# Kernel optimization log

Hardware: AMD Instinct MI355X
Metric: run time of the kernel (lower is better)

Reference implementation:

```python
import jax, jax.numpy as jnp
import numpy as np

N = 100000
E = 800000
HID = 128
HEADS = 4
NEG_SLOPE = 0.2


def _mlp2(x, w1, b1, w2, b2):
    h = jax.nn.relu(x @ w1.T + b1)
    return jax.nn.relu(h @ w2.T + b2)


def gat_conv(h, src, dst, lin_w, att_src, att_dst, bias, heads, out_ch, concat):
    # h: [N, in] -> hl: [N, heads, out_ch]
    n = h.shape[0]
    hl = (h @ lin_w.T).reshape(n, heads, out_ch)
    a_s = jnp.sum(hl * att_src, axis=-1)  # [N, heads]
    a_d = jnp.sum(hl * att_dst, axis=-1)
    alpha = jax.nn.leaky_relu(a_s[src] + a_d[dst], NEG_SLOPE)  # [E', heads]
    amax = jax.ops.segment_max(alpha, dst, num_segments=n)
    ex = jnp.exp(alpha - amax[dst])
    denom = jax.ops.segment_sum(ex, dst, num_segments=n)
    att = ex / denom[dst]  # segment softmax over incoming edges
    msg = hl[src] * att[:, :, None]  # [E', heads, out_ch]
    out = jax.ops.segment_sum(msg, dst, num_segments=n)
    out = out.reshape(n, heads * out_ch) if concat else out.mean(axis=1)
    return out + bias


def setup_inputs() -> dict:
    key = jax.random.key(0)
    ks = iter(jax.random.split(key, 40))
    g = lambda shape: (jax.random.normal(next(ks), shape, dtype=jnp.float32) * 0.1)
    inp = {}
    inp['x'] = jax.random.normal(next(ks), (N, 2), dtype=jnp.float32)
    inp['node_types'] = jax.random.randint(next(ks), (N,), 0, 2, dtype=jnp.int32)
    inp['edge_index'] = jax.random.randint(next(ks), (2, E), 0, N, dtype=jnp.int64)
    # heterogeneous encoder
    inp['ew1'] = g((HID, 2)); inp['eb1'] = g((HID,))
    inp['ew2'] = g((HID, HID)); inp['eb2'] = g((HID,))
    inp['cw1'] = g((HID, 1)); inp['cb1'] = g((HID,))
    inp['cw2'] = g((HID, HID)); inp['cb2'] = g((HID,))
    # GAT layers 0,1: heads=4, out_ch=HID//4, concat
    C = HID // HEADS
    inp['lin0'] = g((HID, HID)); inp['as0'] = g((HEADS, C)); inp['ad0'] = g((HEADS, C)); inp['b0'] = g((HID,))
    inp['lin1'] = g((HID, HID)); inp['as1'] = g((HEADS, C)); inp['ad1'] = g((HEADS, C)); inp['b1'] = g((HID,))
    # GAT layer 2: heads=1, out_ch=HID, concat=False
    inp['lin2'] = g((HID, HID)); inp['as2'] = g((1, HID)); inp['ad2'] = g((1, HID)); inp['b2'] = g((HID,))
    # decoder
    inp['dw1'] = g((HID, HID)); inp['db1'] = g((HID,))
    inp['dw2'] = g((HID // 2, HID)); inp['db2'] = g((HID // 2,))
    inp['dw3'] = g((1, HID // 2)); inp['db3'] = g((1,))
    return inp


def reference(x, node_types, edge_index, ew1, eb1, ew2, eb2, cw1, cb1, cw2, cb2,
              lin0, as0, ad0, b0, lin1, as1, ad1, b1, lin2, as2, ad2, b2,
              dw1, db1, dw2, db2, dw3, db3):
    n = x.shape[0]
    # heterogeneous encoding (vectorized type select)
    item_h = _mlp2(x[:, :2], ew1, eb1, ew2, eb2)
    con_h = _mlp2(x[:, :1], cw1, cb1, cw2, cb2)
    item_mask = node_types == 0
    h = jnp.where(item_mask[:, None], item_h, jnp.where((node_types == 1)[:, None], con_h, 0.0))
    # add self-loops (PyG GATConv default add_self_loops=True)
    loop = jnp.arange(n, dtype=edge_index.dtype)
    src = jnp.concatenate([edge_index[0], loop])
    dst = jnp.concatenate([edge_index[1], loop])
    C = HID // HEADS
    h0 = jax.nn.relu(gat_conv(h, src, dst, lin0, as0, ad0, b0, HEADS, C, True))
    h1 = h0 + jax.nn.relu(gat_conv(h0, src, dst, lin1, as1, ad1, b1, HEADS, C, True))
    h2 = h1 + jax.nn.relu(gat_conv(h1, src, dst, lin2, as2, ad2, b2, 1, HID, False))
    # decoder on all nodes; zero out non-item nodes (dropout is eval/no-op)
    d = jax.nn.relu(h2 @ dw1.T + db1)
    d = jax.nn.relu(d @ dw2.T + db2)
    probs = jax.nn.sigmoid(d @ dw3.T + db3).squeeze(-1)
    return probs * item_mask.astype(probs.dtype)
```

## Files before the change

kernel.cpp:

```cpp
#include <hip/hip_runtime.h>
#include <math.h>

#define HIDDEN 128
#define NEG_SLOPE 0.2f

typedef unsigned short u16;
typedef __attribute__((ext_vector_type(8))) short bf16x8;
typedef __attribute__((ext_vector_type(4))) float f32x4;

__device__ __forceinline__ u16 f2bf(float f) {
    unsigned u = __float_as_uint(f);
    unsigned r = (u + 0x7FFFu + ((u >> 16) & 1u)) >> 16;
    return (u16)r;
}
__device__ __forceinline__ float bf2f(u16 u) {
    return __uint_as_float((unsigned)u << 16);
}
__device__ __forceinline__ unsigned pack2(float a, float b) {
    return (unsigned)f2bf(a) | ((unsigned)f2bf(b) << 16);
}
__device__ __forceinline__ float lo16f(unsigned v) { return bf2f((u16)v); }
__device__ __forceinline__ float hi16f(unsigned v) { return bf2f((u16)(v >> 16)); }

struct WPtrs { const float* p[7]; };
__global__ void convw_zero_kernel(WPtrs wp, unsigned* __restrict__ wb, int totalPairs,
                                  int* __restrict__ cnt, int N) {
    int i = blockIdx.x * blockDim.x + threadIdx.x;
    if (i < N) cnt[i] = 0;
    if (i < totalPairs) {
        int e = i * 2;
        int seg, off;
        if (e < 98304) { seg = e >> 14; off = e & 16383; }
        else           { seg = 6;       off = e - 98304; }
        const float* s = wp.p[seg];
        wb[i] = pack2(s[off], s[off + 1]);
    }
}

__global__ __launch_bounds__(256) void encoder_kernel(
        const float* __restrict__ x, const int* __restrict__ types,
        const float* __restrict__ ew1, const float* __restrict__ eb1,
        const float* __restrict__ cw1, const float* __restrict__ cb1,
        const u16* __restrict__ wb_ew2, const u16* __restrict__ wb_cw2,
        const float* __restrict__ eb2, const float* __restrict__ cb2,
        u16* __restrict__ out, int N) {
    __shared__ u16 Ws[128 * 136];
    __shared__ float xsh[128];
    __shared__ float w1sh[640];
    const int tid = threadIdx.x;
    const int n0 = blockIdx.x * 64;

    if (tid < 128) {
        int n = n0 + (tid >> 1);
        xsh[tid] = (n < N) ? x[2 * n + (tid & 1)] : 0.f;
    }
    if (tid < 256) w1sh[tid] = ew1[tid];
    if (tid < 128) { w1sh[256 + tid] = eb1[tid]; w1sh[384 + tid] = cw1[tid];
                     w1sh[512 + tid] = cb1[tid]; }
#pragma unroll
    for (int r = 0; r < 8; r++) {
        int j = r * 256 + tid;
        int row = j >> 4, c8 = (j & 15) << 3;
        *(uint4*)&Ws[row * 136 + c8] = *(const uint4*)&wb_ew2[(size_t)row * 128 + c8];
    }
    __syncthreads();

    const int w = tid >> 6, lane = tid & 63;
    const int qd = lane >> 4, lr = lane & 15;
    const int arow = w * 16 + lr;
    const float x0 = xsh[2 * arow], x1 = xsh[2 * arow + 1];

    f32x4 acc_i[8], acc_c[8];
#pragma unroll
    for (int j = 0; j < 8; j++) acc_i[j] = (f32x4){0.f, 0.f, 0.f, 0.f};

#pragma unroll
    for (int k = 0; k < 4; k++) {
        bf16x8 a;
#pragma unroll
        for (int j = 0; j < 8; j++) {
            int t = k * 32 + qd * 8 + j;
            float v = fmaxf(w1sh[2 * t] * x0 + w1sh[2 * t + 1] * x1 + w1sh[256 + t], 0.f);
            a[j] = (short)f2bf(v);
        }
#pragma unroll
        for (int j = 0; j < 8; j++) {
            bf16x8 b = *(const bf16x8*)&Ws[(j * 16 + lr) * 136 + k * 32 + qd * 8];
            acc_i[j] = __builtin_amdgcn_mfma_f32_16x16x32_bf16(a, b, acc_i[j], 0, 0, 0);
        }
    }
    __syncthreads();

#pragma unroll
    for (int r = 0; r < 8; r++) {
        int j = r * 256 + tid;
        int rw = j >> 4, c8 = (j & 15) << 3;
        *(uint4*)&Ws[rw * 136 + c8] = *(const uint4*)&wb_cw2[(size_t)rw * 128 + c8];
    }
    __syncthreads();

#pragma unroll
    for (int j = 0; j < 8; j++) acc_c[j] = (f32x4){0.f, 0.f, 0.f, 0.f};
#pragma unroll
    for (int k = 0; k < 4; k++) {
        bf16x8 a;
#pragma unroll
        for (int j = 0; j < 8; j++) {
            int t = k * 32 + qd * 8 + j;
            float v = fmaxf(w1sh[384 + t] * x0 + w1sh[512 + t], 0.f);
            a[j] = (short)f2bf(v);
        }
#pragma unroll
        for (int j = 0; j < 8; j++) {
            bf16x8 b = *(const bf16x8*)&Ws[(j * 16 + lr) * 136 + k * 32 + qd * 8];
            acc_c[j] = __builtin_amdgcn_mfma_f32_16x16x32_bf16(a, b, acc_c[j], 0, 0, 0);
        }
    }

#pragma unroll
    for (int r = 0; r < 4; r++) {
        int orow = n0 + w * 16 + qd * 4 + r;
        if (orow >= N) continue;
        int ty = types[orow];
#pragma unroll
        for (int j = 0; j < 8; j++) {
            int col = j * 16 + lr;
            float v;
            if (ty == 0)      v = fmaxf(acc_i[j][r] + eb2[col], 0.f);
            else if (ty == 1) v = fmaxf(acc_c[j][r] + cb2[col], 0.f);
            else              v = 0.f;
            out[(size_t)orow * HIDDEN + col] = f2bf(v);
        }
    }
}

template <int DH>
__global__ __launch_bounds__(256) void gemm_hl_kernel(
        const u16* __restrict__ X, const u16* __restrict__ Wb,
        const float* __restrict__ att_s, const float* __restrict__ att_d,
        u16* __restrict__ hl, float* __restrict__ a_s, float* __restrict__ a_d,
        int N) {
    __shared__ u16 Xs[64 * 136];
    __shared__ u16 Ws[128 * 136];
    const int tid = threadIdx.x;
    const int n0 = blockIdx.x * 64;

#pragma unroll
    for (int r = 0; r < 4; r++) {
        int j = r * 256 + tid;
        int row = j >> 4, c8 = (j & 15) << 3;
        int n = n0 + row;
        uint4 v = make_uint4(0u, 0u, 0u, 0u);
        if (n < N) v = *(const uint4*)&X[(size_t)n * 128 + c8];
        *(uint4*)&Xs[row * 136 + c8] = v;
    }
#pragma unroll
    for (int r = 0; r < 8; r++) {
        int j = r * 256 + tid;
        int row = j >> 4, c8 = (j & 15) << 3;
        *(uint4*)&Ws[row * 136 + c8] = *(const uint4*)&Wb[(size_t)row * 128 + c8];
    }
    __syncthreads();

    const int w = tid >> 6, lane = tid & 63;
    const int qd = lane >> 4, lr = lane & 15;

    f32x4 acc[8];
#pragma unroll
    for (int j = 0; j < 8; j++) acc[j] = (f32x4){0.f, 0.f, 0.f, 0.f};
#pragma unroll
    for (int k = 0; k < 4; k++) {
        bf16x8 a = *(const bf16x8*)&Xs[(w * 16 + lr) * 136 + k * 32 + qd * 8];
#pragma unroll
        for (int j = 0; j < 8; j++) {
            bf16x8 b = *(const bf16x8*)&Ws[(j * 16 + lr) * 136 + k * 32 + qd * 8];
            acc[j] = __builtin_amdgcn_mfma_f32_16x16x32_bf16(a, b, acc[j], 0, 0, 0);
        }
    }

    constexpr int NH = (DH == 4) ? 4 : 1;
    float sp[NH][4], dp[NH][4];
#pragma unroll
    for (int h = 0; h < NH; h++)
#pragma unroll
        for (int r = 0; r < 4; r++) { sp[h][r] = 0.f; dp[h][r] = 0.f; }
#pragma unroll
    for (int j = 0; j < 8; j++) {
        int col = j * 16 + lr;
        float as_ = att_s[col], ad_ = att_d[col];
        int h = (DH == 4) ? (j >> 1) : 0;
#pragma unroll
        for (int r = 0; r < 4; r++) {
            sp[h][r] += acc[j][r] * as_;
            dp[h][r] += acc[j][r] * ad_;
        }
    }
#pragma unroll
    for (int m = 1; m < 16; m <<= 1)
#pragma unroll
        for (int h = 0; h < NH; h++)
#pragma unroll
            for (int r = 0; r < 4; r++) {
                sp[h][r] += __shfl_xor(sp[h][r], m, 64);
                dp[h][r] += __shfl_xor(dp[h][r], m, 64);
            }
    if (lr == 0) {
#pragma unroll
        for (int r = 0; r < 4; r++) {
            int row = n0 + w * 16 + qd * 4 + r;
            if (row < N) {
#pragma unroll
                for (int h = 0; h < NH; h++) {
                    a_s[row * DH + h] = sp[h][r];
                    a_d[row * DH + h] = dp[h][r];
                }
            }
        }
    }
#pragma unroll
    for (int r = 0; r < 4; r++) {
        int row = n0 + w * 16 + qd * 4 + r;
        if (row >= N) continue;
#pragma unroll
        for (int j = 0; j < 8; j++)
            hl[(size_t)row * 128 + j * 16 + lr] = f2bf(acc[j][r]);
    }
}

__global__ __launch_bounds__(256) void dec_kernel(
        const u16* __restrict__ X, const int* __restrict__ types,
        const u16* __restrict__ wb_dw1, const float* __restrict__ db1,
        const u16* __restrict__ wb_dw2, const float* __restrict__ db2,
        const float* __restrict__ dw3, const float* __restrict__ db3,
        float* __restrict__ fout, int N) {
    __shared__ u16 Xs[64 * 136];
    __shared__ u16 Ws[128 * 136];
    const int tid = threadIdx.x;
    const int n0 = blockIdx.x * 64;

#pragma unroll
    for (int r = 0; r < 4; r++) {
        int j = r * 256 + tid;
        int row = j >> 4, c8 = (j & 15) << 3;
        int n = n0 + row;
        uint4 v = make_uint4(0u, 0u, 0u, 0u);
        if (n < N) v = *(const uint4*)&X[(size_t)n * 128 + c8];
        *(uint4*)&Xs[row * 136 + c8] = v;
    }
#pragma unroll
    for (int r = 0; r < 8; r++) {
        int j = r * 256 + tid;
        int row = j >> 4, c8 = (j & 15) << 3;
        *(uint4*)&Ws[row * 136 + c8] = *(const uint4*)&wb_dw1[(size_t)row * 128 + c8];
    }
    __syncthreads();

    const int w = tid >> 6, lane = tid & 63;
    const int qd = lane >> 4, lr = lane & 15;

    f32x4 acc[8];
#pragma unroll
    for (int j = 0; j < 8; j++) acc[j] = (f32x4){0.f, 0.f, 0.f, 0.f};
#pragma unroll
    for (int k = 0; k < 4; k++) {
        bf16x8 a = *(const bf16x8*)&Xs[(w * 16 + lr) * 136 + k * 32 + qd * 8];
#pragma unroll
        for (int j = 0; j < 8; j++) {
            bf16x8 b = *(const bf16x8*)&Ws[(j * 16 + lr) * 136 + k * 32 + qd * 8];
            acc[j] = __builtin_amdgcn_mfma_f32_16x16x32_bf16(a, b, acc[j], 0, 0, 0);
        }
    }
    __syncthreads();

#pragma unroll
    for (int r = 0; r < 4; r++) {
        int drow = w * 16 + qd * 4 + r;
#pragma unroll
        for (int j = 0; j < 8; j++) {
            int col = j * 16 + lr;
            float v = fmaxf(acc[j][r] + db1[col], 0.f);
            float vo = __shfl_xor(v, 1, 64);
            if ((lr & 1) == 0)
                *(unsigned*)&Xs[drow * 136 + j * 16 + lr] = pack2(v, vo);
        }
    }
#pragma unroll
    for (int r = 0; r < 4; r++) {
        int j = r * 256 + tid;
        int row = j >> 4, c8 = (j & 15) << 3;
        *(uint4*)&Ws[row * 136 + c8] = *(const uint4*)&wb_dw2[(size_t)row * 128 + c8];
    }
    __syncthreads();

    f32x4 acc2[4];
#pragma unroll
    for (int j = 0; j < 4; j++) acc2[j] = (f32x4){0.f, 0.f, 0.f, 0.f};
#pragma unroll
    for (int k = 0; k < 4; k++) {
        bf16x8 a = *(const bf16x8*)&Xs[(w * 16 + lr) * 136 + k * 32 + qd * 8];
#pragma unroll
        for (int j = 0; j < 4; j++) {
            bf16x8 b = *(const bf16x8*)&Ws[(j * 16 + lr) * 136 + k * 32 + qd * 8];
            acc2[j] = __builtin_amdgcn_mfma_f32_16x16x32_bf16(a, b, acc2[j], 0, 0, 0);
        }
    }
    float pr[4] = {0.f, 0.f, 0.f, 0.f};
#pragma unroll
    for (int j = 0; j < 4; j++) {
        int col = j * 16 + lr;
        float b = db2[col], wv = dw3[col];
#pragma unroll
        for (int r = 0; r < 4; r++) pr[r] += fmaxf(acc2[j][r] + b, 0.f) * wv;
    }
#pragma unroll
    for (int m = 1; m < 16; m <<= 1)
#pragma unroll
        for (int r = 0; r < 4; r++) pr[r] += __shfl_xor(pr[r], m, 64);
    if (lr == 0) {
        float b3 = db3[0];
#pragma unroll
        for (int r = 0; r < 4; r++) {
            int row = n0 + w * 16 + qd * 4 + r;
            if (row < N) {
                float prob = 1.f / (1.f + expf(-(pr[r] + b3)));
                fout[row] = (types[row] == 0) ? prob : 0.f;
            }
        }
    }
}

__global__ void hist_kernel(const int* __restrict__ ei, int E, int E2,
                            int* __restrict__ cnt, int* __restrict__ pos) {
    int e = blockIdx.x * blockDim.x + threadIdx.x;
    if (e >= E2) return;
    int d = (e < E) ? ei[E + e] : e - E;
    pos[e] = atomicAdd(&cnt[d], 1);
}

__global__ void scan1_kernel(const int* __restrict__ cnt, int* __restrict__ rs,
                             int* __restrict__ bsum, int N) {
    __shared__ int s[256];
    int i = blockIdx.x * 256 + threadIdx.x;
    int v = (i < N) ? cnt[i] : 0;
    s[threadIdx.x] = v;
    __syncthreads();
    for (int off = 1; off < 256; off <<= 1) {
        int t = (threadIdx.x >= off) ? s[threadIdx.x - off] : 0;
        __syncthreads();
        s[threadIdx.x] += t;
        __syncthreads();
    }
    if (i < N) rs[i] = s[threadIdx.x];
    if (threadIdx.x == 255) bsum[blockIdx.x] = s[255];
}

__global__ void scan23_kernel(int* __restrict__ rs, const int* __restrict__ cnt,
                              const int* __restrict__ bsum, int N) {
    __shared__ int sdata[256];
    int b = blockIdx.x;
    int partial = 0;
    for (int i = threadIdx.x; i < b; i += 256) partial += bsum[i];
    sdata[threadIdx.x] = partial;
    __syncthreads();
    for (int off = 128; off; off >>= 1) {
        if (threadIdx.x < off) sdata[threadIdx.x] += sdata[threadIdx.x + off];
        __syncthreads();
    }
    int pre = sdata[0];
    int i = b * 256 + threadIdx.x;
    if (i < N) rs[i] = rs[i] - cnt[i] + pre;
}

__global__ void scatter_kernel(const int* __restrict__ ei, int E, int E2,
                               const int* __restrict__ rs, const int* __restrict__ pos,
                               int* __restrict__ srclist) {
    int e = blockIdx.x * blockDim.x + threadIdx.x;
    if (e >= E2) return;
    int s, d;
    if (e < E) { s = ei[e]; d = ei[E + e]; }
    else       { s = d = e - E; }
    srclist[rs[d] + pos[e]] = s;
}

template <int H>
__global__ __launch_bounds__(256) void gat_agg_kernel(
        const int* __restrict__ rs, const int* __restrict__ cnt,
        const int* __restrict__ srclist, const u16* __restrict__ hl,
        const float* __restrict__ a_s, const float* __restrict__ a_d,
        const float* __restrict__ bias, const u16* __restrict__ res,
        u16* __restrict__ out, int N) {
    int n = blockIdx.x * 4 + (threadIdx.x >> 6);
    int l = threadIdx.x & 63;
    if (n >= N) return;
    const int g = l >> 4;
    const int c = l & 15;
    const int head = (H == 1) ? 0 : (c >> 2);
    const int beg = rs[n];
    const int deg = cnt[n];
    const float ad = a_d[n * H + head];
    float acc0[8], acc1[8], acc2[8];
    float den0 = 0.f, den1 = 0.f, den2 = 0.f;
#pragma unroll
    for (int j = 0; j < 8; j++) { acc0[j] = 0.f; acc1[j] = 0.f; acc2[j] = 0.f; }

    for (int k = 0; k < deg; k += 12) {
        int i0 = k + g, i1 = k + 4 + g, i2 = k + 8 + g;
        int e0 = beg + min(i0, deg - 1);
        int e1 = beg + min(i1, deg - 1);
        int e2 = beg + min(i2, deg - 1);
        int s0 = srclist[e0], s1 = srclist[e1], s2 = srclist[e2];
        float al0 = a_s[s0 * H + head] + ad;
        float al1 = a_s[s1 * H + head] + ad;
        float al2 = a_s[s2 * H + head] + ad;
        al0 = (al0 > 0.f) ? al0 : NEG_SLOPE * al0;
        al1 = (al1 > 0.f) ? al1 : NEG_SLOPE * al1;
        al2 = (al2 > 0.f) ? al2 : NEG_SLOPE * al2;
        float p0 = __expf(fminf(al0, 80.f));
        float p1 = __expf(fminf(al1, 80.f));
        float p2 = __expf(fminf(al2, 80.f));
        if (i0 >= deg) p0 = 0.f;
        if (i1 >= deg) p1 = 0.f;
        if (i2 >= deg) p2 = 0.f;
        den0 += p0; den1 += p1; den2 += p2;
        uint4 v0 = *(const uint4*)&hl[(size_t)s0 * 128 + 8 * c];
        uint4 v1 = *(const uint4*)&hl[(size_t)s1 * 128 + 8 * c];
        uint4 v2 = *(const uint4*)&hl[(size_t)s2 * 128 + 8 * c];
        acc0[0] += p0 * lo16f(v0.x); acc0[1] += p0 * hi16f(v0.x);
        acc0[2] += p0 * lo16f(v0.y); acc0[3] += p0 * hi16f(v0.y);
        acc0[4] += p0 * lo16f(v0.z); acc0[5] += p0 * hi16f(v0.z);
        acc0[6] += p0 * lo16f(v0.w); acc0[7] += p0 * hi16f(v0.w);
        acc1[0] += p1 * lo16f(v1.x); acc1[1] += p1 * hi16f(v1.x);
        acc1[2] += p1 * lo16f(v1.y); acc1[3] += p1 * hi16f(v1.y);
        acc1[4] += p1 * lo16f(v1.z); acc1[5] += p1 * hi16f(v1.z);
        acc1[6] += p1 * lo16f(v1.w); acc1[7] += p1 * hi16f(v1.w);
        acc2[0] += p2 * lo16f(v2.x); acc2[1] += p2 * hi16f(v2.x);
        acc2[2] += p2 * lo16f(v2.y); acc2[3] += p2 * hi16f(v2.y);
        acc2[4] += p2 * lo16f(v2.z); acc2[5] += p2 * hi16f(v2.z);
        acc2[6] += p2 * lo16f(v2.w); acc2[7] += p2 * hi16f(v2.w);
    }
#pragma unroll
    for (int j = 0; j < 8; j++) {
        float a = acc0[j] + acc1[j] + acc2[j];
        a += __shfl_xor(a, 16, 64);
        a += __shfl_xor(a, 32, 64);
        acc0[j] = a;
    }
    float den = den0 + den1 + den2;
    den += __shfl_xor(den, 16, 64);
    den += __shfl_xor(den, 32, 64);
    if (g == 0) {
        float di = 1.f / den;
        float4 b0 = *(const float4*)&bias[8 * c];
        float4 b1 = *(const float4*)&bias[8 * c + 4];
        float o[8];
        o[0] = fmaxf(acc0[0] * di + b0.x, 0.f);
        o[1] = fmaxf(acc0[1] * di + b0.y, 0.f);
        o[2] = fmaxf(acc0[2] * di + b0.z, 0.f);
        o[3] = fmaxf(acc0[3] * di + b0.w, 0.f);
        o[4] = fmaxf(acc0[4] * di + b1.x, 0.f);
        o[5] = fmaxf(acc0[5] * di + b1.y, 0.f);
        o[6] = fmaxf(acc0[6] * di + b1.z, 0.f);
        o[7] = fmaxf(acc0[7] * di + b1.w, 0.f);
        if (res) {
            uint4 rv = *(const uint4*)&res[(size_t)n * 128 + 8 * c];
            o[0] += lo16f(rv.x); o[1] += hi16f(rv.x);
            o[2] += lo16f(rv.y); o[3] += hi16f(rv.y);
            o[4] += lo16f(rv.z); o[5] += hi16f(rv.z);
            o[6] += lo16f(rv.w); o[7] += hi16f(rv.w);
        }
        uint4 ov = make_uint4(pack2(o[0], o[1]), pack2(o[2], o[3]),
                              pack2(o[4], o[5]), pack2(o[6], o[7]));
        *(uint4*)&out[(size_t)n * 128 + 8 * c] = ov;
    }
}

extern "C" void kernel_launch(void* const* d_in, const int* in_sizes, int n_in,
                              void* d_out, int out_size, void* d_ws, size_t ws_size,
                              hipStream_t stream) {
    const float* x     = (const float*)d_in[0];
    const int*   types = (const int*)d_in[1];
    const int*   ei    = (const int*)d_in[2];
    const float* ew1 = (const float*)d_in[3];
    const float* eb1 = (const float*)d_in[4];
    const float* ew2 = (const float*)d_in[5];
    const float* eb2 = (const float*)d_in[6];
    const float* cw1 = (const float*)d_in[7];
    const float* cb1 = (const float*)d_in[8];
    const float* cw2 = (const float*)d_in[9];
    const float* cb2 = (const float*)d_in[10];
    const float* lin0 = (const float*)d_in[11];
    const float* as0  = (const float*)d_in[12];
    const float* ad0  = (const float*)d_in[13];
    const float* b0   = (const float*)d_in[14];
    const float* lin1 = (const float*)d_in[15];
    const float* as1  = (const float*)d_in[16];
    const float* ad1  = (const float*)d_in[17];
    const float* b1   = (const float*)d_in[18];
    const float* lin2 = (const float*)d_in[19];
    const float* as2  = (const float*)d_in[20];
    const float* ad2  = (const float*)d_in[21];
    const float* b2   = (const float*)d_in[22];
    const float* dw1 = (const float*)d_in[23];
    const float* db1 = (const float*)d_in[24];
    const float* dw2 = (const float*)d_in[25];
    const float* db2 = (const float*)d_in[26];
    const float* dw3 = (const float*)d_in[27];
    const float* db3 = (const float*)d_in[28];

    int N  = in_sizes[1];
    int E  = in_sizes[2] / 2;
    int E2 = E + N;

    size_t NF = (size_t)N * HIDDEN;
    u16* bufA = (u16*)d_ws;
    u16* bufB = bufA + NF;
    u16* bufC = bufB + NF;
    float* a_s  = (float*)(bufC + NF);
    float* a_d  = a_s + (size_t)N * 4;
    int* rs      = (int*)(a_d + (size_t)N * 4);
    int* cnt     = rs + N;
    int* pos     = cnt + N;
    int* bsum    = pos + E2;
    int* srclist = bsum + 1024;
    u16* wb      = (u16*)(srclist + E2);
    u16* wb_ew2  = wb;
    u16* wb_cw2  = wb + 16384;
    u16* wb_lin0 = wb + 32768;
    u16* wb_lin1 = wb + 49152;
    u16* wb_lin2 = wb + 65536;
    u16* wb_dw1  = wb + 81920;
    u16* wb_dw2  = wb + 98304;

    int nb = (N + 255) / 256;

    WPtrs wp;
    wp.p[0] = ew2; wp.p[1] = cw2; wp.p[2] = lin0; wp.p[3] = lin1;
    wp.p[4] = lin2; wp.p[5] = dw1; wp.p[6] = dw2;
    int cz = max(N, 53248);
    convw_zero_kernel<<<(cz + 255) / 256, 256, 0, stream>>>(wp, (unsigned*)wb, 53248,
                                                            cnt, N);

    hist_kernel<<<(E2 + 255) / 256, 256, 0, stream>>>(ei, E, E2, cnt, pos);
    scan1_kernel<<<nb, 256, 0, stream>>>(cnt, rs, bsum, N);
    scan23_kernel<<<nb, 256, 0, stream>>>(rs, cnt, bsum, N);
    scatter_kernel<<<(E2 + 255) / 256, 256, 0, stream>>>(ei, E, E2, rs, pos, srclist);

    int gx = (N + 63) / 64;

    encoder_kernel<<<gx, 256, 0, stream>>>(x, types, ew1, eb1, cw1, cb1,
                                           wb_ew2, wb_cw2, eb2, cb2, bufA, N);

    gemm_hl_kernel<4><<<gx, 256, 0, stream>>>(bufA, wb_lin0, as0, ad0,
                                              bufB, a_s, a_d, N);
    gat_agg_kernel<4><<<(N + 3) / 4, 256, 0, stream>>>(rs, cnt, srclist, bufB,
                                                       a_s, a_d, b0, nullptr, bufA, N);
    gemm_hl_kernel<4><<<gx, 256, 0, stream>>>(bufA, wb_lin1, as1, ad1,
                                              bufB, a_s, a_d, N);
    gat_agg_kernel<4><<<(N + 3) / 4, 256, 0, stream>>>(rs, cnt, srclist, bufB,
                                                       a_s, a_d, b1, bufA, bufC, N);
    gemm_hl_kernel<1><<<gx, 256, 0, stream>>>(bufC, wb_lin2, as2, ad2,
                                              bufB, a_s, a_d, N);
    gat_agg_kernel<1><<<(N + 3) / 4, 256, 0, stream>>>(rs, cnt, srclist, bufB,
                                                       a_s, a_d, b2, bufC, bufA, N);

    dec_kernel<<<gx, 256, 0, stream>>>(bufA, types, wb_dw1, db1, wb_dw2, db2,
                                       dw3, db3, (float*)d_out, N);
}
```

Before: 470.0 us.

## Co-schedule CSR histogram and scan blocks inside encoder and first GEMM launches

The edge histogram is merged into the encoder launch as extra blocks, and the first-level scan into the first GEMM launch as extra blocks. Independent graph-preprocessing work can then run alongside the dense kernels, and two launches are dropped. The cost is that the fused kernels carry extra block-index branches. The scan blocks also inherit the GEMM's larger shared-memory allocation, which may lower occupancy for those blocks.

```diff
diff --git a/kernel.cpp b/kernel.cpp
--- a/kernel.cpp
+++ b/kernel.cpp
@@ -37,13 +37,23 @@
     }
 }
 
-__global__ __launch_bounds__(256) void encoder_kernel(
+__global__ __launch_bounds__(256) void enc_hist_kernel(
         const float* __restrict__ x, const int* __restrict__ types,
         const float* __restrict__ ew1, const float* __restrict__ eb1,
         const float* __restrict__ cw1, const float* __restrict__ cb1,
         const u16* __restrict__ wb_ew2, const u16* __restrict__ wb_cw2,
         const float* __restrict__ eb2, const float* __restrict__ cb2,
-        u16* __restrict__ out, int N) {
+        u16* __restrict__ out, int N, int encBlocks,
+        const int* __restrict__ ei, int E, int E2,
+        int* __restrict__ cnt, int* __restrict__ pos) {
+    if ((int)blockIdx.x >= encBlocks) {
+        int e = (blockIdx.x - encBlocks) * 256 + threadIdx.x;
+        if (e < E2) {
+            int d = (e < E) ? ei[E + e] : e - E;
+            pos[e] = atomicAdd(&cnt[d], 1);
+        }
+        return;
+    }
     __shared__ u16 Ws[128 * 136];
     __shared__ float xsh[128];
     __shared__ float w1sh[640];
@@ -139,12 +149,31 @@
         const u16* __restrict__ X, const u16* __restrict__ Wb,
         const float* __restrict__ att_s, const float* __restrict__ att_d,
         u16* __restrict__ hl, float* __restrict__ a_s, float* __restrict__ a_d,
-        int N) {
+        int N, int gemmBlocks,
+        const int* __restrict__ cnt, int* __restrict__ rs, int* __restrict__ bsum) {
     __shared__ u16 Xs[64 * 136];
     __shared__ u16 Ws[128 * 136];
     const int tid = threadIdx.x;
+
+    if ((int)blockIdx.x >= gemmBlocks) {
+        int* s = (int*)Xs;
+        int chunk = blockIdx.x - gemmBlocks;
+        int i = chunk * 256 + tid;
+        int v = (i < N) ? cnt[i] : 0;
+        s[tid] = v;
+        __syncthreads();
+        for (int off = 1; off < 256; off <<= 1) {
+            int t = (tid >= off) ? s[tid - off] : 0;
+            __syncthreads();
+            s[tid] += t;
+            __syncthreads();
+        }
+        if (i < N) rs[i] = s[tid];
+        if (tid == 255) bsum[chunk] = s[255];
+        return;
+    }
+
     const int n0 = blockIdx.x * 64;
-
 #pragma unroll
     for (int r = 0; r < 4; r++) {
         int j = r * 256 + tid;
@@ -327,31 +356,6 @@
             }
         }
     }
-}
-
-__global__ void hist_kernel(const int* __restrict__ ei, int E, int E2,
-                            int* __restrict__ cnt, int* __restrict__ pos) {
-    int e = blockIdx.x * blockDim.x + threadIdx.x;
-    if (e >= E2) return;
-    int d = (e < E) ? ei[E + e] : e - E;
-    pos[e] = atomicAdd(&cnt[d], 1);
-}
-
-__global__ void scan1_kernel(const int* __restrict__ cnt, int* __restrict__ rs,
-                             int* __restrict__ bsum, int N) {
-    __shared__ int s[256];
-    int i = blockIdx.x * 256 + threadIdx.x;
-    int v = (i < N) ? cnt[i] : 0;
-    s[threadIdx.x] = v;
-    __syncthreads();
-    for (int off = 1; off < 256; off <<= 1) {
-        int t = (threadIdx.x >= off) ? s[threadIdx.x - off] : 0;
-        __syncthreads();
-        s[threadIdx.x] += t;
-        __syncthreads();
-    }
-    if (i < N) rs[i] = s[threadIdx.x];
-    if (threadIdx.x == 255) bsum[blockIdx.x] = s[255];
 }
 
 __global__ void scan23_kernel(int* __restrict__ rs, const int* __restrict__ cnt,
@@ -532,6 +536,8 @@
     u16* wb_dw2  = wb + 98304;
 
     int nb = (N + 255) / 256;
+    int hb = (E2 + 255) / 256;
+    int gx = (N + 63) / 64;
 
     WPtrs wp;
     wp.p[0] = ew2; wp.p[1] = cw2; wp.p[2] = lin0; wp.p[3] = lin1;
@@ -540,26 +546,26 @@
     convw_zero_kernel<<<(cz + 255) / 256, 256, 0, stream>>>(wp, (unsigned*)wb, 53248,
                                                             cnt, N);
 
-    hist_kernel<<<(E2 + 255) / 256, 256, 0, stream>>>(ei, E, E2, cnt, pos);
-    scan1_kernel<<<nb, 256, 0, stream>>>(cnt, rs, bsum, N);
+    enc_hist_kernel<<<gx + hb, 256, 0, stream>>>(x, types, ew1, eb1, cw1, cb1,
+                                                 wb_ew2, wb_cw2, eb2, cb2, bufA, N,
+                                                 gx, ei, E, E2, cnt, pos);
+
+    gemm_hl_kernel<4><<<gx + nb, 256, 0, stream>>>(bufA, wb_lin0, as0, ad0,
+                                                   bufB, a_s, a_d, N, gx,
+                                                   cnt, rs, bsum);
     scan23_kernel<<<nb, 256, 0, stream>>>(rs, cnt, bsum, N);
-    scatter_kernel<<<(E2 + 255) / 256, 256, 0, stream>>>(ei, E, E2, rs, pos, srclist);
-
-    int gx = (N + 63) / 64;
-
-    encoder_kernel<<<gx, 256, 0, stream>>>(x, types, ew1, eb1, cw1, cb1,
-                                           wb_ew2, wb_cw2, eb2, cb2, bufA, N);
-
-    gemm_hl_kernel<4><<<gx, 256, 0, stream>>>(bufA, wb_lin0, as0, ad0,
-                                              bufB, a_s, a_d, N);
+    scatter_kernel<<<hb, 256, 0, stream>>>(ei, E, E2, rs, pos, srclist);
+
     gat_agg_kernel<4><<<(N + 3) / 4, 256, 0, stream>>>(rs, cnt, srclist, bufB,
                                                        a_s, a_d, b0, nullptr, bufA, N);
     gemm_hl_kernel<4><<<gx, 256, 0, stream>>>(bufA, wb_lin1, as1, ad1,
-                                              bufB, a_s, a_d, N);
+                                              bufB, a_s, a_d, N, gx,
+                                              nullptr, nullptr, nullptr);
     gat_agg_kernel<4><<<(N + 3) / 4, 256, 0, stream>>>(rs, cnt, srclist, bufB,
                                                        a_s, a_d, b1, bufA, bufC, N);
     gemm_hl_kernel<1><<<gx, 256, 0, stream>>>(bufC, wb_lin2, as2, ad2,
-                                              bufB, a_s, a_d, N);
+                                              bufB, a_s, a_d, N, gx,
+                                              nullptr, nullptr, nullptr);
     gat_agg_kernel<1><<<(N + 3) / 4, 256, 0, stream>>>(rs, cnt, srclist, bufB,
                                                        a_s, a_d, b2, bufC, bufA, N);
 
```

Result: faster. 455.6 us (-3.1%).
